# Performance work log

Hardware: AMD Instinct MI355X
Metric: run time of the kernel (lower is better)

## Reference

```python
import jax, jax.numpy as jnp
import numpy as np

N, C_IN, C_OUT, T, V = 64, 128, 128, 128, 25
REL = C_IN // 8  # rel_channels = 16


def setup_inputs() -> dict:
    key = jax.random.key(0)
    ks = jax.random.split(key, 12)
    s_in = 1.0 / np.sqrt(C_IN)
    s_rel = 1.0 / np.sqrt(REL)
    return {
        "x": jax.random.normal(ks[0], (N, C_IN, T, V), jnp.float32),
        "A": jax.random.normal(ks[1], (V, V), jnp.float32),
        "alpha": jnp.float32(1.0),
        "W1": jax.random.normal(ks[2], (REL, C_IN), jnp.float32) * s_in,
        "b1": jnp.zeros((REL,), jnp.float32),
        "W2": jax.random.normal(ks[3], (REL, C_IN), jnp.float32) * s_in,
        "b2": jnp.zeros((REL,), jnp.float32),
        "W3": jax.random.normal(ks[4], (C_OUT, C_IN), jnp.float32) * s_in,
        "b3": jnp.zeros((C_OUT,), jnp.float32),
        "W4": jax.random.normal(ks[5], (C_OUT, REL), jnp.float32) * s_rel,
        "b4": jnp.zeros((C_OUT,), jnp.float32),
    }


def reference(x, A, alpha, W1, b1, W2, b2, W3, b3, W4, b4):
    # conv1(x).mean(-2) and conv2(x).mean(-2): 1x1 conv is linear, so mean over
    # T commutes with it -> compute mean first to avoid an (N,REL,T,V) temp.
    xm = x.mean(axis=2)                                        # (N, C, V)
    x1 = jnp.einsum('rc,ncv->nrv', W1, xm) + b1[None, :, None]  # (N, R, V)
    x2 = jnp.einsum('rc,ncv->nrv', W2, xm) + b2[None, :, None]  # (N, R, V)
    x3 = jnp.einsum('oc,nctv->notv', W3, x) + b3[None, :, None, None]  # (N,O,T,V)
    # tanh of broadcasted pairwise difference: (N, R, V, V)
    d = jnp.tanh(x1[:, :, :, None] - x2[:, :, None, :])
    # conv4 (1x1 over channel dim) -> learned per-channel adjacency
    adj = jnp.einsum('or,nrvu->novu', W4, d) + b4[None, :, None, None]
    adj = adj * alpha + A[None, None, :, :]                    # (N, O, V, V)
    return jnp.einsum('ncvu,nctv->nctu', adj, x3)              # (N, O, T, V)
```

## Files before the change

### kernel.cpp

```cpp
#include <hip/hip_runtime.h>


#define NB   64
#define CIN  128
#define COUT 128
#define TT   128
#define VV   25
#define REL  16

#define JT 25
#define KT 4
#define XF_BYTES (JT * KT * 1024)
#define X3_STRIDE 1040
#define LDS_BYTES (COUT * X3_STRIDE)
#define TSTRIDE 416

typedef __attribute__((ext_vector_type(8))) short bf16x8;
typedef __attribute__((ext_vector_type(4))) float f32x4;

__device__ inline short f2bf(float f) {
    unsigned u = __float_as_uint(f);
    u += 0x7fff + ((u >> 16) & 1);
    return (short)(u >> 16);
}

__launch_bounds__(256)
__global__ void k_prep(const float* __restrict__ x, float* __restrict__ xm,
                       char* __restrict__ Xf) {
    __shared__ float tile[32 * TSTRIDE];
    int tid = threadIdx.x;
    int kt = blockIdx.x >> 3, tb = blockIdx.x & 7, n = blockIdx.y;
    int c0 = kt * 32;

    const float* src = x + (size_t)(n * CIN + c0) * 3200 + tb * 400;
#pragma unroll
    for (int p = 0; p < 13; ++p) {
        int i = tid + p * 256;
        if (i < 3200) {
            int c = i / 100, q = i - c * 100;
            int sw = ((c >> 3) & 1) << 4;
            *reinterpret_cast<float4*>(&tile[c * TSTRIDE + ((q * 4) ^ sw)]) =
                *reinterpret_cast<const float4*>(src + (size_t)c * 3200 + q * 4);
        }
    }
    __syncthreads();

#pragma unroll
    for (int pp = 0; pp < 4; ++pp) {
        int p = tid + pp * 256;
        if (p < 800) {
            int c = p / 25, v = p - c * 25;
            int sw = ((c >> 3) & 1) << 4;
            float s = 0.f;
#pragma unroll
            for (int t = 0; t < 16; ++t) s += tile[c * TSTRIDE + ((t * 25 + v) ^ sw)];
            atomicAdd(&xm[((size_t)n * CIN + c0 + c) * VV + v], s * (1.0f / TT));
        }
    }

    char* dst = Xf + (size_t)(n * 8 + tb) * XF_BYTES + (size_t)kt * 25600;
    for (int ch = tid; ch < 1600; ch += 256) {
        int l = ch & 63, jt = ch >> 6;
        int j = jt * 16 + (l & 15);
        int cl = 8 * (l >> 4);
        int sw = ((l >> 4) & 1) << 4;
        bf16x8 v;
#pragma unroll
        for (int b = 0; b < 8; ++b)
            v[b] = f2bf(tile[(cl + b) * TSTRIDE + (j ^ sw)]);
        *reinterpret_cast<bf16x8*>(dst + (size_t)ch * 16) = v;
    }
}

__global__ void k_adj(const float* __restrict__ xm,
                      const float* __restrict__ A, const float* __restrict__ alphap,
                      const float* __restrict__ W1, const float* __restrict__ b1,
                      const float* __restrict__ W2, const float* __restrict__ b2,
                      const float* __restrict__ W4, const float* __restrict__ b4,
                      const float* __restrict__ W3, char* __restrict__ W3f,
                      char* __restrict__ adjT) {
    __shared__ char adjS[32 * 2048];
    __shared__ float xms[CIN * VV];
    __shared__ float W1s[REL * CIN];
    __shared__ float W2s[REL * CIN];
    __shared__ float x1s[REL * VV];
    __shared__ float x2s[REL * VV];
    __shared__ float W4s[32 * REL];
    __shared__ float b4s[32];

    int tid = threadIdx.x;
    int n = blockIdx.x;
    int o0 = blockIdx.y * 32;

    if (n == 0) {
#pragma unroll
        for (int pass = 0; pass < 2; ++pass) {
            int chunk = blockIdx.y * 512 + pass * 256 + tid;
            int l = chunk & 63;
            int frag = chunk >> 6;
            int ct = frag >> 2, kt = frag & 3;
            int c = ct * 16 + (l & 15);
            int kb = kt * 32 + 8 * (l >> 4);
            const float4 f0 = *reinterpret_cast<const float4*>(&W3[(size_t)c * CIN + kb]);
            const float4 f1 = *reinterpret_cast<const float4*>(&W3[(size_t)c * CIN + kb + 4]);
            bf16x8 vv;
            vv[0] = f2bf(f0.x); vv[1] = f2bf(f0.y); vv[2] = f2bf(f0.z); vv[3] = f2bf(f0.w);
            vv[4] = f2bf(f1.x); vv[5] = f2bf(f1.y); vv[6] = f2bf(f1.z); vv[7] = f2bf(f1.w);
            *reinterpret_cast<bf16x8*>(W3f + (size_t)chunk * 16) = vv;
        }
    }

    for (int i = tid; i < 16384; i += 256) reinterpret_cast<float*>(adjS)[i] = 0.f;
    for (int i = tid; i < CIN * VV; i += 256) xms[i] = xm[(size_t)n * CIN * VV + i];
    for (int i = tid; i < REL * CIN; i += 256) { W1s[i] = W1[i]; W2s[i] = W2[i]; }
    for (int i = tid; i < 32 * REL; i += 256) W4s[i] = W4[o0 * REL + i];
    if (tid < 32) b4s[tid] = b4[o0 + tid];
    __syncthreads();

    for (int task = tid; task < 2 * REL * VV; task += 256) {
        int rv = task % (REL * VV);
        int which = task / (REL * VV);
        int r = rv / VV, v = rv % VV;
        const float* Ws = which ? W2s : W1s;
        float s = 0.f;
#pragma unroll 8
        for (int c = 0; c < CIN; ++c) s = fmaf(Ws[r * CIN + c], xms[c * VV + v], s);
        s += which ? b2[r] : b1[r];
        (which ? x2s : x1s)[rv] = s;
    }
    __syncthreads();

    float alpha = alphap[0];
    for (int p = tid; p < VV * VV; p += 256) {
        int v = p / VV, u = p % VV;
        float d[REL];
#pragma unroll
        for (int r = 0; r < REL; ++r) d[r] = tanhf(x1s[r * VV + v] - x2s[r * VV + u]);
        float Avu = A[v * VV + u];
        int off = (u >> 4) * 1024 + (((u & 15) + 16 * (v >> 3)) * 16) + (v & 7) * 2;
        for (int oo = 0; oo < 32; ++oo) {
            float s = 0.f;
#pragma unroll
            for (int r = 0; r < REL; ++r) s = fmaf(W4s[oo * REL + r], d[r], s);
            float val = alpha * (s + b4s[oo]) + Avu;
            *(short*)(adjS + oo * 2048 + off) = f2bf(val);
        }
    }
    __syncthreads();

    float4* dst = reinterpret_cast<float4*>(adjT + (size_t)(n * COUT + o0) * 2048);
    const float4* src = reinterpret_cast<const float4*>(adjS);
    for (int i = tid; i < 4096; i += 256) dst[i] = src[i];
}

__launch_bounds__(1024)
__global__ void k_main(const char* __restrict__ Xf, const char* __restrict__ W3f,
                       const float* __restrict__ b3, const char* __restrict__ adjT,
                       float* __restrict__ out) {
    __shared__ __align__(16) char lds[LDS_BYTES];

    int tid = threadIdx.x;
    int tb = blockIdx.x, n = blockIdx.y;
    int lane = tid & 63, w = tid >> 6;
    int g = lane >> 4, lr = lane & 15;
    int ct = w >> 1, jh = w & 1;
    int jt0 = jh ? 13 : 0;
    int njt = jh ? 12 : 13;

    const char* xfb = Xf + (size_t)(n * 8 + tb) * XF_BYTES;
#pragma unroll
    for (int q = 0; q < 7; ++q) {
        int chunk = tid + q * 1024;
        if (chunk < JT * KT * 64)
            *reinterpret_cast<bf16x8*>(lds + (size_t)chunk * 16) =
                *reinterpret_cast<const bf16x8*>(xfb + (size_t)chunk * 16);
    }
    __syncthreads();

    f32x4 acc[13];
#pragma unroll
    for (int u = 0; u < 13; ++u) acc[u] = f32x4{0.f, 0.f, 0.f, 0.f};
#pragma unroll
    for (int kt = 0; kt < KT; ++kt) {
        bf16x8 a = *reinterpret_cast<const bf16x8*>(
            W3f + (size_t)((ct * 4 + kt) * 64 + lane) * 16);
#pragma unroll
        for (int u = 0; u < 13; ++u) {
            if (u < njt) {
                int jt = jt0 + u;
                bf16x8 bx = *reinterpret_cast<const bf16x8*>(
                    lds + (size_t)((kt * JT + jt) * 64 + lane) * 16);
                acc[u] = __builtin_amdgcn_mfma_f32_16x16x32_bf16(a, bx, acc[u], 0, 0, 0);
            }
        }
    }
    __syncthreads();

    int cbase = ct * 16 + 4 * g;
    float bv[4];
#pragma unroll
    for (int r = 0; r < 4; ++r) bv[r] = b3[cbase + r];
#pragma unroll
    for (int u = 0; u < 13; ++u) {
        if (u < njt) {
            int j = (jt0 + u) * 16 + lr;
            int t = j / 25, v = j - t * 25;
            int off = (t + 16 * (v >> 3)) * 16 + (v & 7) * 2;
#pragma unroll
            for (int r = 0; r < 4; ++r)
                *(short*)(lds + (size_t)(cbase + r) * X3_STRIDE + off) =
                    f2bf(acc[u][r] + bv[r]);
        }
    }
#pragma unroll
    for (int z = 0; z < 14; ++z) {
        int idx = tid + z * 1024;
        int c = idx / 112;
        int rem = idx - c * 112;
        int t = rem / 7, qq = rem - t * 7;
        *(short*)(lds + (size_t)c * X3_STRIDE + (t + 48) * 16 + 2 + qq * 2) = 0;
    }
    __syncthreads();

    const char* adjTb = adjT + (size_t)(n * COUT) * 2048;
    int t0 = tb * 16;
#pragma unroll
    for (int cc = 0; cc < 8; ++cc) {
        int c = w * 8 + cc;
        bf16x8 a = *reinterpret_cast<const bf16x8*>(lds + (size_t)c * X3_STRIDE + lane * 16);
        const bf16x8* bp = reinterpret_cast<const bf16x8*>(adjTb + (size_t)c * 2048);
        bf16x8 b0 = bp[lane];
        bf16x8 b1 = bp[64 + lane];
        f32x4 z = {0.f, 0.f, 0.f, 0.f};
        f32x4 d0 = __builtin_amdgcn_mfma_f32_16x16x32_bf16(a, b0, z, 0, 0, 0);
        f32x4 d1 = __builtin_amdgcn_mfma_f32_16x16x32_bf16(a, b1, z, 0, 0, 0);
        float* ob = out + ((size_t)(n * COUT + c) * TT + t0) * VV;
#pragma unroll
        for (int rr = 0; rr < 4; ++rr) {
            int t = 4 * g + rr;
            ob[(size_t)t * VV + lr] = d0[rr];
            if (lr < 9) ob[(size_t)t * VV + 16 + lr] = d1[rr];
        }
    }
}

extern "C" void kernel_launch(void* const* d_in, const int* in_sizes, int n_in,
                              void* d_out, int out_size, void* d_ws, size_t ws_size,
                              hipStream_t stream) {
    const float* x     = (const float*)d_in[0];
    const float* A     = (const float*)d_in[1];
    const float* alpha = (const float*)d_in[2];
    const float* W1    = (const float*)d_in[3];
    const float* b1    = (const float*)d_in[4];
    const float* W2    = (const float*)d_in[5];
    const float* b2    = (const float*)d_in[6];
    const float* W3    = (const float*)d_in[7];
    const float* b3    = (const float*)d_in[8];
    const float* W4    = (const float*)d_in[9];
    const float* b4    = (const float*)d_in[10];
    float* out = (float*)d_out;

    float* xm  = (float*)d_ws;
    char* adjT = (char*)d_ws + 819200;
    char* W3f  = (char*)d_ws + 819200 + 16777216;
    char* Xf   = (char*)d_ws + 819200 + 16777216 + 32768;

    hipMemsetAsync(xm, 0, 819200, stream);
    k_prep<<<dim3(32, NB), 256, 0, stream>>>(x, xm, Xf);
    k_adj<<<dim3(NB, 4), 256, 0, stream>>>(xm, A, alpha, W1, b1, W2, b2, W4, b4,
                                           W3, W3f, adjT);
    k_main<<<dim3(TT / 16, NB), 1024, 0, stream>>>(Xf, W3f, b3, adjT, out);
}
```

Measured before the change: 124.8 us.

## Split main kernel over output-channel halves and replace atomic mean with partial planes

The main kernel now runs 512-thread blocks over a third grid dimension that splits output channels into two halves. The Xf tile is streamed through a smaller 51 KB LDS buffer in two K-halves, and the x3 staging is done in four chunks through a scratch area. LDS use per block drops from about 133 KB to 51 KB, so more blocks can be resident per CU, at the cost of loading the Xf tile twice (once per channel half) and adding extra barriers. Separately, k_prep writes per-time-block partial sums into eight planes instead of using atomicAdd, and k_adj sums them, which removes the memset and the atomics.

Result: slower. 161.9 us (+29.7%).

```diff
diff --git a/kernel.cpp b/kernel.cpp
--- a/kernel.cpp
+++ b/kernel.cpp
@@ -11,9 +11,11 @@
 #define JT 25
 #define KT 4
 #define XF_BYTES (JT * KT * 1024)
-#define X3_STRIDE 1040
-#define LDS_BYTES (COUT * X3_STRIDE)
+#define XH_BYTES 51200
+#define SCR_STRIDE 1040
+#define LDS_BYTES 51200
 #define TSTRIDE 416
+#define XMP_PLANE (NB * CIN * VV)
 
 typedef __attribute__((ext_vector_type(8))) short bf16x8;
 typedef __attribute__((ext_vector_type(4))) float f32x4;
@@ -25,7 +27,7 @@
 }
 
 __launch_bounds__(256)
-__global__ void k_prep(const float* __restrict__ x, float* __restrict__ xm,
+__global__ void k_prep(const float* __restrict__ x, float* __restrict__ xmp,
                        char* __restrict__ Xf) {
     __shared__ float tile[32 * TSTRIDE];
     int tid = threadIdx.x;
@@ -54,7 +56,7 @@
             float s = 0.f;
 #pragma unroll
             for (int t = 0; t < 16; ++t) s += tile[c * TSTRIDE + ((t * 25 + v) ^ sw)];
-            atomicAdd(&xm[((size_t)n * CIN + c0 + c) * VV + v], s * (1.0f / TT));
+            xmp[(size_t)tb * XMP_PLANE + ((size_t)n * CIN + c0 + c) * VV + v] = s;
         }
     }
 
@@ -72,7 +74,7 @@
     }
 }
 
-__global__ void k_adj(const float* __restrict__ xm,
+__global__ void k_adj(const float* __restrict__ xmp,
                       const float* __restrict__ A, const float* __restrict__ alphap,
                       const float* __restrict__ W1, const float* __restrict__ b1,
                       const float* __restrict__ W2, const float* __restrict__ b2,
@@ -111,7 +113,13 @@
     }
 
     for (int i = tid; i < 16384; i += 256) reinterpret_cast<float*>(adjS)[i] = 0.f;
-    for (int i = tid; i < CIN * VV; i += 256) xms[i] = xm[(size_t)n * CIN * VV + i];
+    for (int i = tid; i < CIN * VV; i += 256) {
+        float s = 0.f;
+#pragma unroll
+        for (int tb = 0; tb < 8; ++tb)
+            s += xmp[(size_t)tb * XMP_PLANE + (size_t)n * CIN * VV + i];
+        xms[i] = s * (1.0f / TT);
+    }
     for (int i = tid; i < REL * CIN; i += 256) { W1s[i] = W1[i]; W2s[i] = W2[i]; }
     for (int i = tid; i < 32 * REL; i += 256) W4s[i] = W4[o0 * REL + i];
     if (tid < 32) b4s[tid] = b4[o0 + tid];
@@ -153,94 +161,109 @@
     for (int i = tid; i < 4096; i += 256) dst[i] = src[i];
 }
 
-__launch_bounds__(1024)
+__launch_bounds__(512, 6)
 __global__ void k_main(const char* __restrict__ Xf, const char* __restrict__ W3f,
                        const float* __restrict__ b3, const char* __restrict__ adjT,
                        float* __restrict__ out) {
     __shared__ __align__(16) char lds[LDS_BYTES];
 
     int tid = threadIdx.x;
-    int tb = blockIdx.x, n = blockIdx.y;
+    int tb = blockIdx.x, n = blockIdx.y, ch = blockIdx.z;
     int lane = tid & 63, w = tid >> 6;
     int g = lane >> 4, lr = lane & 15;
-    int ct = w >> 1, jh = w & 1;
+    int ctl = w >> 1, jh = w & 1;
+    int ct = ch * 4 + ctl;
     int jt0 = jh ? 13 : 0;
     int njt = jh ? 12 : 13;
 
     const char* xfb = Xf + (size_t)(n * 8 + tb) * XF_BYTES;
-#pragma unroll
-    for (int q = 0; q < 7; ++q) {
-        int chunk = tid + q * 1024;
-        if (chunk < JT * KT * 64)
-            *reinterpret_cast<bf16x8*>(lds + (size_t)chunk * 16) =
-                *reinterpret_cast<const bf16x8*>(xfb + (size_t)chunk * 16);
-    }
-    __syncthreads();
 
     f32x4 acc[13];
 #pragma unroll
     for (int u = 0; u < 13; ++u) acc[u] = f32x4{0.f, 0.f, 0.f, 0.f};
-#pragma unroll
-    for (int kt = 0; kt < KT; ++kt) {
-        bf16x8 a = *reinterpret_cast<const bf16x8*>(
-            W3f + (size_t)((ct * 4 + kt) * 64 + lane) * 16);
+
+#pragma unroll
+    for (int h = 0; h < 2; ++h) {
+#pragma unroll
+        for (int q = 0; q < 7; ++q) {
+            int chunk = tid + q * 512;
+            if (chunk < 3200)
+                *reinterpret_cast<bf16x8*>(lds + (size_t)chunk * 16) =
+                    *reinterpret_cast<const bf16x8*>(
+                        xfb + (size_t)h * XH_BYTES + (size_t)chunk * 16);
+        }
+        __syncthreads();
+#pragma unroll
+        for (int kk = 0; kk < 2; ++kk) {
+            int kt = h * 2 + kk;
+            bf16x8 a = *reinterpret_cast<const bf16x8*>(
+                W3f + (size_t)((ct * 4 + kt) * 64 + lane) * 16);
+#pragma unroll
+            for (int u = 0; u < 13; ++u) {
+                if (u < njt) {
+                    int jt = jt0 + u;
+                    bf16x8 bx = *reinterpret_cast<const bf16x8*>(
+                        lds + (size_t)((kk * JT + jt) * 64 + lane) * 16);
+                    acc[u] = __builtin_amdgcn_mfma_f32_16x16x32_bf16(a, bx, acc[u], 0, 0, 0);
+                }
+            }
+        }
+        __syncthreads();
+    }
+
+#pragma unroll
+    for (int z = 0; z < 4; ++z) {
+        int idx = tid + z * 512;
+        if (idx < 16 * 112) {
+            int s = idx / 112;
+            int rem = idx - s * 112;
+            int t = rem / 7, qq = rem - t * 7;
+            *(short*)(lds + (size_t)s * SCR_STRIDE + (t + 48) * 16 + 2 + qq * 2) = 0;
+        }
+    }
+
+    float bv[4];
+#pragma unroll
+    for (int r = 0; r < 4; ++r) bv[r] = b3[ct * 16 + 4 * g + r];
+
+    const char* adjTb = adjT + (size_t)(n * COUT) * 2048;
+    int t0 = tb * 16;
+
+#pragma unroll
+    for (int ck = 0; ck < 4; ++ck) {
 #pragma unroll
         for (int u = 0; u < 13; ++u) {
             if (u < njt) {
-                int jt = jt0 + u;
-                bf16x8 bx = *reinterpret_cast<const bf16x8*>(
-                    lds + (size_t)((kt * JT + jt) * 64 + lane) * 16);
-                acc[u] = __builtin_amdgcn_mfma_f32_16x16x32_bf16(a, bx, acc[u], 0, 0, 0);
+                int j = (jt0 + u) * 16 + lr;
+                int t = j / 25, v = j - t * 25;
+                int off = (t + 16 * (v >> 3)) * 16 + (v & 7) * 2;
+                *(short*)(lds + (size_t)(ctl * 4 + g) * SCR_STRIDE + off) =
+                    f2bf(acc[u][ck] + bv[ck]);
             }
         }
-    }
-    __syncthreads();
-
-    int cbase = ct * 16 + 4 * g;
-    float bv[4];
-#pragma unroll
-    for (int r = 0; r < 4; ++r) bv[r] = b3[cbase + r];
-#pragma unroll
-    for (int u = 0; u < 13; ++u) {
-        if (u < njt) {
-            int j = (jt0 + u) * 16 + lr;
-            int t = j / 25, v = j - t * 25;
-            int off = (t + 16 * (v >> 3)) * 16 + (v & 7) * 2;
-#pragma unroll
-            for (int r = 0; r < 4; ++r)
-                *(short*)(lds + (size_t)(cbase + r) * X3_STRIDE + off) =
-                    f2bf(acc[u][r] + bv[r]);
-        }
-    }
-#pragma unroll
-    for (int z = 0; z < 14; ++z) {
-        int idx = tid + z * 1024;
-        int c = idx / 112;
-        int rem = idx - c * 112;
-        int t = rem / 7, qq = rem - t * 7;
-        *(short*)(lds + (size_t)c * X3_STRIDE + (t + 48) * 16 + 2 + qq * 2) = 0;
-    }
-    __syncthreads();
-
-    const char* adjTb = adjT + (size_t)(n * COUT) * 2048;
-    int t0 = tb * 16;
-#pragma unroll
-    for (int cc = 0; cc < 8; ++cc) {
-        int c = w * 8 + cc;
-        bf16x8 a = *reinterpret_cast<const bf16x8*>(lds + (size_t)c * X3_STRIDE + lane * 16);
-        const bf16x8* bp = reinterpret_cast<const bf16x8*>(adjTb + (size_t)c * 2048);
-        bf16x8 b0 = bp[lane];
-        bf16x8 b1 = bp[64 + lane];
-        f32x4 z = {0.f, 0.f, 0.f, 0.f};
-        f32x4 d0 = __builtin_amdgcn_mfma_f32_16x16x32_bf16(a, b0, z, 0, 0, 0);
-        f32x4 d1 = __builtin_amdgcn_mfma_f32_16x16x32_bf16(a, b1, z, 0, 0, 0);
-        float* ob = out + ((size_t)(n * COUT + c) * TT + t0) * VV;
-#pragma unroll
-        for (int rr = 0; rr < 4; ++rr) {
-            int t = 4 * g + rr;
-            ob[(size_t)t * VV + lr] = d0[rr];
-            if (lr < 9) ob[(size_t)t * VV + 16 + lr] = d1[rr];
-        }
+        __syncthreads();
+
+#pragma unroll
+        for (int i = 0; i < 2; ++i) {
+            int s = 2 * w + i;
+            int c = (ch * 4 + (s >> 2)) * 16 + (s & 3) * 4 + ck;
+            bf16x8 a = *reinterpret_cast<const bf16x8*>(
+                lds + (size_t)s * SCR_STRIDE + lane * 16);
+            const bf16x8* bp = reinterpret_cast<const bf16x8*>(adjTb + (size_t)c * 2048);
+            bf16x8 b0 = bp[lane];
+            bf16x8 b1 = bp[64 + lane];
+            f32x4 z = {0.f, 0.f, 0.f, 0.f};
+            f32x4 d0 = __builtin_amdgcn_mfma_f32_16x16x32_bf16(a, b0, z, 0, 0, 0);
+            f32x4 d1 = __builtin_amdgcn_mfma_f32_16x16x32_bf16(a, b1, z, 0, 0, 0);
+            float* ob = out + ((size_t)(n * COUT + c) * TT + t0) * VV;
+#pragma unroll
+            for (int rr = 0; rr < 4; ++rr) {
+                int t = 4 * g + rr;
+                ob[(size_t)t * VV + lr] = d0[rr];
+                if (lr < 9) ob[(size_t)t * VV + 16 + lr] = d1[rr];
+            }
+        }
+        __syncthreads();
     }
 }
 
@@ -260,14 +283,13 @@
     const float* b4    = (const float*)d_in[10];
     float* out = (float*)d_out;
 
-    float* xm  = (float*)d_ws;
-    char* adjT = (char*)d_ws + 819200;
-    char* W3f  = (char*)d_ws + 819200 + 16777216;
-    char* Xf   = (char*)d_ws + 819200 + 16777216 + 32768;
-
-    hipMemsetAsync(xm, 0, 819200, stream);
-    k_prep<<<dim3(32, NB), 256, 0, stream>>>(x, xm, Xf);
-    k_adj<<<dim3(NB, 4), 256, 0, stream>>>(xm, A, alpha, W1, b1, W2, b2, W4, b4,
+    float* xmp = (float*)d_ws;
+    char* adjT = (char*)d_ws + 6553600;
+    char* W3f  = (char*)d_ws + 6553600 + 16777216;
+    char* Xf   = (char*)d_ws + 6553600 + 16777216 + 32768;
+
+    k_prep<<<dim3(32, NB), 256, 0, stream>>>(x, xmp, Xf);
+    k_adj<<<dim3(NB, 4), 256, 0, stream>>>(xmp, A, alpha, W1, b1, W2, b2, W4, b4,
                                            W3, W3f, adjT);
-    k_main<<<dim3(TT / 16, NB), 1024, 0, stream>>>(Xf, W3f, b3, adjT, out);
-}
+    k_main<<<dim3(TT / 16, NB, 2), 512, 0, stream>>>(Xf, W3f, b3, adjT, out);
+}
```
